# Performance work log

Hardware: AMD Instinct MI355X
Metric: run time of the kernel (lower is better)

Reference implementation:

```python
import jax, jax.numpy as jnp
import numpy as np

B, F = 64, 2048

def setup_inputs() -> dict:
    key = jax.random.key(0)
    k1, k2, k3, k4, k5 = jax.random.split(key, 5)
    scale = 1.0 / np.sqrt(F)
    return {
        "x": jax.random.normal(k1, (B, F), dtype=jnp.float32),
        "feature_mask": jax.random.randint(k2, (B, F), 0, 2, dtype=jnp.int32),
        "Wq": jax.random.normal(k3, (F, F), dtype=jnp.float32) * scale,
        "Wk": jax.random.normal(k4, (F, F), dtype=jnp.float32) * scale,
        "Wv": jax.random.normal(k5, (F, F), dtype=jnp.float32) * scale,
    }

def reference(x, feature_mask, Wq, Wk, Wv):
    # nn.Linear(bias=False): y = x @ W.T
    q = x @ Wq.T  # (B, F)
    k = x @ Wk.T
    v = x @ Wv.T
    # outer-product scores: (B, F, F) = q[:, :, None] * k[:, None, :]
    scores = q[:, :, None] * k[:, None, :]
    # mask broadcast over query dim (unsqueeze(1) in torch)
    scores = jnp.where(feature_mask[:, None, :] == 0, -1e9, scores)
    attn = jax.nn.softmax(scores, axis=-1)  # (B, F, F)
    attended = jnp.einsum("bfg,bg->bf", attn, v)  # (B, F)
    return attended
```

## Files before the change

### kernel.cpp

```cpp
#include <hip/hip_runtime.h>
#include <hip/hip_bf16.h>

#define B 64
#define F 2048
#define BN 32
#define BK 32
#define KSPLIT 4
#define KCHUNK (F / KSPLIT)
#define NITER (KCHUNK / BK)
#define LDSW 40
#define GS 4

typedef __attribute__((ext_vector_type(8))) short bf16x8;
typedef __attribute__((ext_vector_type(4))) float f32x4;

#define PART_FLOATS (KSPLIT * 3 * B * F)

#if __has_builtin(__builtin_amdgcn_exp2f)
#define EXP2(x) __builtin_amdgcn_exp2f(x)
#else
#define EXP2(x) exp2f(x)
#endif

__device__ __forceinline__ void split2(float f0, float f1, int& hi, int& lo) {
  union { float f; unsigned u; } a, b;
  a.f = f0; b.f = f1;
  union { unsigned u; float f; } ha, hb;
  ha.u = a.u & 0xFFFF0000u;
  hb.u = b.u & 0xFFFF0000u;
  union { float f; unsigned u; } la, lb;
  la.f = f0 - ha.f;
  lb.f = f1 - hb.f;
  hi = (int)__builtin_amdgcn_perm(b.u, a.u, 0x07060302u);
  lo = (int)__builtin_amdgcn_perm(lb.u, la.u, 0x07060302u);
}

__global__ __launch_bounds__(256) void qkv_gemm_kernel(
    const float* __restrict__ x, const float* __restrict__ Wq,
    const float* __restrict__ Wk, const float* __restrict__ Wv,
    float* __restrict__ part) {
  __shared__ __align__(16) short xs_hi[2][B][LDSW];
  __shared__ __align__(16) short xs_lo[2][B][LDSW];
  __shared__ __align__(16) short ws_hi[2][BN][LDSW];
  __shared__ __align__(16) short ws_lo[2][BN][LDSW];

  const int tid  = threadIdx.x;
  const int f0   = blockIdx.x * BN;
  const int kb   = blockIdx.y;
  const int mat  = blockIdx.z;
  const float* W = (mat == 0) ? Wq : (mat == 1) ? Wk : Wv;

  const int lrow = tid >> 2;
  const int lc0  = (tid & 3) << 3;
  const int wrow = tid >> 3;
  const int wc0  = (tid & 7) << 2;

  const int wave = tid >> 6;
  const int lane = tid & 63;
  const int l15  = lane & 15;
  const int quad = lane >> 4;

  const float* xg = x + lrow * F + kb * KCHUNK + lc0;
  const float* wg = W + (f0 + wrow) * F + kb * KCHUNK + wc0;

  f32x4 acc[2];
#pragma unroll
  for (int i = 0; i < 2; ++i) acc[i] = (f32x4){0.f, 0.f, 0.f, 0.f};

  float4 px[2][2], pw[2];
  px[0][0] = *(const float4*)(xg);
  px[0][1] = *(const float4*)(xg + 4);
  pw[0]    = *(const float4*)(wg);

#pragma unroll
  for (int it = 0; it < NITER; ++it) {
    const int cur = it & 1, nxt = cur ^ 1;
    if (it + 1 < NITER) {
      const float* xp = xg + (it + 1) * BK;
      px[nxt][0] = *(const float4*)(xp);
      px[nxt][1] = *(const float4*)(xp + 4);
      pw[nxt]    = *(const float4*)(wg + (it + 1) * BK);
    }
    int4 xh, xl;
    int2 wh, wl;
    split2(px[cur][0].x, px[cur][0].y, xh.x, xl.x);
    split2(px[cur][0].z, px[cur][0].w, xh.y, xl.y);
    split2(px[cur][1].x, px[cur][1].y, xh.z, xl.z);
    split2(px[cur][1].z, px[cur][1].w, xh.w, xl.w);
    split2(pw[cur].x, pw[cur].y, wh.x, wl.x);
    split2(pw[cur].z, pw[cur].w, wh.y, wl.y);
    *(int4*)&xs_hi[cur][lrow][lc0] = xh;
    *(int4*)&xs_lo[cur][lrow][lc0] = xl;
    *(int2*)&ws_hi[cur][wrow][wc0] = wh;
    *(int2*)&ws_lo[cur][wrow][wc0] = wl;
    __syncthreads();

    bf16x8 a_hi = *(const bf16x8*)&xs_hi[cur][(wave << 4) + l15][quad << 3];
    bf16x8 a_lo = *(const bf16x8*)&xs_lo[cur][(wave << 4) + l15][quad << 3];
#pragma unroll
    for (int nt = 0; nt < 2; ++nt) {
      bf16x8 b_hi = *(const bf16x8*)&ws_hi[cur][(nt << 4) + l15][quad << 3];
      bf16x8 b_lo = *(const bf16x8*)&ws_lo[cur][(nt << 4) + l15][quad << 3];
      acc[nt] = __builtin_amdgcn_mfma_f32_16x16x32_bf16(a_hi, b_hi, acc[nt], 0, 0, 0);
      acc[nt] = __builtin_amdgcn_mfma_f32_16x16x32_bf16(a_hi, b_lo, acc[nt], 0, 0, 0);
      acc[nt] = __builtin_amdgcn_mfma_f32_16x16x32_bf16(a_lo, b_hi, acc[nt], 0, 0, 0);
    }
  }

  float* outp = part + (size_t)(kb * 3 + mat) * B * F;
#pragma unroll
  for (int nt = 0; nt < 2; ++nt) {
    int f = f0 + (nt << 4) + l15;
#pragma unroll
    for (int r = 0; r < 4; ++r) {
      int brow = (wave << 4) + (quad << 2) + r;
      outp[brow * F + f] = acc[nt][r];
    }
  }
}

__global__ __launch_bounds__(1024, 8) void attn_kernel(
    const float* __restrict__ part, const int* __restrict__ mask,
    float* __restrict__ out) {
  __shared__ __align__(16) float kvs[2 * F];
  __shared__ float rn[GS][256];
  __shared__ float rd[GS][256];
  __shared__ float swv[16], swm[16], swn[16];
  __shared__ int scnt;

  const int b     = blockIdx.x;
  const int tid   = threadIdx.x;
  const int fl    = tid & 255;
  const int slice = __builtin_amdgcn_readfirstlane(tid >> 8);
  const int fi    = blockIdx.y * 256 + fl;
  const int wid   = tid >> 6;
  const int lane  = tid & 63;

  if (tid == 0) scnt = 0;
  __syncthreads();

  float s = 0.f;
#pragma unroll
  for (int p = 0; p < KSPLIT; ++p) s += part[((p * 3 + 0) * B + b) * F + fi];

  const int g0 = tid << 1;
  float2 k2 = {0.f, 0.f}, v2 = {0.f, 0.f};
#pragma unroll
  for (int p = 0; p < KSPLIT; ++p) {
    const float2 kp = *(const float2*)&part[((p * 3 + 1) * B + b) * F + g0];
    const float2 vp = *(const float2*)&part[((p * 3 + 2) * B + b) * F + g0];
    k2.x += kp.x; k2.y += kp.y;
    v2.x += vp.x; v2.y += vp.y;
  }
  float vs = v2.x + v2.y;

  const int2 m2 = *(const int2*)&mask[b * F + g0];
  const bool a0 = (m2.x != 0), a1 = (m2.y != 0);
  const unsigned long long bal0 = __ballot(a0);
  const unsigned long long bal1 = __ballot(a1);
  const int tot = __popcll(bal0) + __popcll(bal1);
  int base = 0;
  if (lane == 0) base = atomicAdd(&scnt, tot);
  base = __shfl(base, 0);

  const unsigned long long ltm = (1ull << lane) - 1ull;
  float kmx = -3.4e38f, kmn = 3.4e38f;
  if (a0) {
    int pos = base + __popcll(bal0 & ltm);
    *(float2*)&kvs[2 * pos] = (float2){k2.x, v2.x};
    kmx = fmaxf(kmx, k2.x); kmn = fminf(kmn, k2.x);
  }
  if (a1) {
    int pos = base + __popcll(bal0) + __popcll(bal1 & ltm);
    *(float2*)&kvs[2 * pos] = (float2){k2.y, v2.y};
    kmx = fmaxf(kmx, k2.y); kmn = fminf(kmn, k2.y);
  }

#pragma unroll
  for (int o = 32; o > 0; o >>= 1) {
    vs += __shfl_xor(vs, o);
    kmx = fmaxf(kmx, __shfl_xor(kmx, o));
    kmn = fminf(kmn, __shfl_xor(kmn, o));
  }
  if (lane == 0) { swv[wid] = vs; swm[wid] = kmx; swn[wid] = kmn; }
  __syncthreads();

  const int ntot = scnt;
  float km = -3.4e38f, kn = 3.4e38f, vstot = 0.f;
#pragma unroll
  for (int w = 0; w < 16; ++w) {
    km = fmaxf(km, swm[w]);
    kn = fminf(kn, swn[w]);
    vstot += swv[w];
  }

  const float L2E = 1.44269504088896f;
  const float se  = s * L2E;
  const float nm2 = -se * ((s >= 0.f) ? km : kn);

  float n0 = 0.f, n1 = 0.f, n2 = 0.f, n3 = 0.f;
  float d0 = 0.f, d1 = 0.f, d2 = 0.f, d3 = 0.f;
  {
    const int quads = ntot >> 1;
    const int q0 = (slice * quads) / GS;
    const int q1 = ((slice + 1) * quads) / GS;
    const float4* bp = (const float4*)kvs;
    int q = q0;
    for (; q + 4 <= q1; q += 4) {
      float4 p0 = bp[q];
      float4 p1 = bp[q + 1];
      float4 p2 = bp[q + 2];
      float4 p3 = bp[q + 3];
      float e0 = EXP2(fmaf(se, p0.x, nm2));
      float e1 = EXP2(fmaf(se, p0.z, nm2));
      float e2 = EXP2(fmaf(se, p1.x, nm2));
      float e3 = EXP2(fmaf(se, p1.z, nm2));
      float e4 = EXP2(fmaf(se, p2.x, nm2));
      float e5 = EXP2(fmaf(se, p2.z, nm2));
      float e6 = EXP2(fmaf(se, p3.x, nm2));
      float e7 = EXP2(fmaf(se, p3.z, nm2));
      n0 = fmaf(e0, p0.y, n0); d0 += e0;
      n1 = fmaf(e1, p0.w, n1); d1 += e1;
      n2 = fmaf(e2, p1.y, n2); d2 += e2;
      n3 = fmaf(e3, p1.w, n3); d3 += e3;
      n0 = fmaf(e4, p2.y, n0); d0 += e4;
      n1 = fmaf(e5, p2.w, n1); d1 += e5;
      n2 = fmaf(e6, p3.y, n2); d2 += e6;
      n3 = fmaf(e7, p3.w, n3); d3 += e7;
    }
    for (; q < q1; ++q) {
      float4 p0 = bp[q];
      float e0 = EXP2(fmaf(se, p0.x, nm2));
      float e1 = EXP2(fmaf(se, p0.z, nm2));
      n0 = fmaf(e0, p0.y, n0); d0 += e0;
      n1 = fmaf(e1, p0.w, n1); d1 += e1;
    }
    if ((slice == GS - 1) && (ntot & 1)) {
      float2 p = *(const float2*)(kvs + 2 * (ntot - 1));
      float e = EXP2(fmaf(se, p.x, nm2));
      n2 = fmaf(e, p.y, n2); d2 += e;
    }
  }
  rn[slice][fl] = (n0 + n1) + (n2 + n3);
  rd[slice][fl] = (d0 + d1) + (d2 + d3);
  __syncthreads();
  if (slice == 0) {
    float N = (rn[0][fl] + rn[1][fl]) + (rn[2][fl] + rn[3][fl]);
    float D = (rd[0][fl] + rd[1][fl]) + (rd[2][fl] + rd[3][fl]);
    out[b * F + fi] = (ntot > 0) ? (N / D) : (vstot * (1.0f / (float)F));
  }
}

extern "C" void kernel_launch(void* const* d_in, const int* in_sizes, int n_in,
                              void* d_out, int out_size, void* d_ws, size_t ws_size,
                              hipStream_t stream) {
  const float* x  = (const float*)d_in[0];
  const int* mask = (const int*)d_in[1];
  const float* Wq = (const float*)d_in[2];
  const float* Wk = (const float*)d_in[3];
  const float* Wv = (const float*)d_in[4];
  float* out = (float*)d_out;

  float* part = (float*)d_ws;

  dim3 gg(F / BN, KSPLIT, 3);
  qkv_gemm_kernel<<<gg, 256, 0, stream>>>(x, Wq, Wk, Wv, part);
  dim3 ga(B, F / 256);
  attn_kernel<<<ga, 1024, 0, stream>>>(part, mask, out);
}
```

Baseline: 121.2 us.

## Register-block four queries per thread and split keys across all sixteen waves

```diff
diff --git a/kernel.cpp b/kernel.cpp
--- a/kernel.cpp
+++ b/kernel.cpp
@@ -9,7 +9,6 @@
 #define KCHUNK (F / KSPLIT)
 #define NITER (KCHUNK / BK)
 #define LDSW 40
-#define GS 4
 
 typedef __attribute__((ext_vector_type(8))) short bf16x8;
 typedef __attribute__((ext_vector_type(4))) float f32x4;
@@ -123,25 +122,28 @@
     const float* __restrict__ part, const int* __restrict__ mask,
     float* __restrict__ out) {
   __shared__ __align__(16) float kvs[2 * F];
-  __shared__ float rn[GS][256];
-  __shared__ float rd[GS][256];
+  __shared__ float rn[16][256];
+  __shared__ float rd[16][256];
   __shared__ float swv[16], swm[16], swn[16];
   __shared__ int scnt;
 
-  const int b     = blockIdx.x;
-  const int tid   = threadIdx.x;
-  const int fl    = tid & 255;
-  const int slice = __builtin_amdgcn_readfirstlane(tid >> 8);
-  const int fi    = blockIdx.y * 256 + fl;
-  const int wid   = tid >> 6;
-  const int lane  = tid & 63;
+  const int b    = blockIdx.x;
+  const int tid  = threadIdx.x;
+  const int wid  = __builtin_amdgcn_readfirstlane(tid >> 6);
+  const int lane = tid & 63;
 
   if (tid == 0) scnt = 0;
   __syncthreads();
 
-  float s = 0.f;
-#pragma unroll
-  for (int p = 0; p < KSPLIT; ++p) s += part[((p * 3 + 0) * B + b) * F + fi];
+  float qsum[4];
+#pragma unroll
+  for (int r = 0; r < 4; ++r) {
+    const int fi = blockIdx.y * 256 + (r << 6) + lane;
+    float s = 0.f;
+#pragma unroll
+    for (int p = 0; p < KSPLIT; ++p) s += part[((p * 3 + 0) * B + b) * F + fi];
+    qsum[r] = s;
+  }
 
   const int g0 = tid << 1;
   float2 k2 = {0.f, 0.f}, v2 = {0.f, 0.f};
@@ -195,59 +197,52 @@
   }
 
   const float L2E = 1.44269504088896f;
-  const float se  = s * L2E;
-  const float nm2 = -se * ((s >= 0.f) ? km : kn);
-
-  float n0 = 0.f, n1 = 0.f, n2 = 0.f, n3 = 0.f;
-  float d0 = 0.f, d1 = 0.f, d2 = 0.f, d3 = 0.f;
+  float se[4], nm[4];
+#pragma unroll
+  for (int r = 0; r < 4; ++r) {
+    se[r] = qsum[r] * L2E;
+    nm[r] = -se[r] * ((qsum[r] >= 0.f) ? km : kn);
+  }
+
+  float n[4] = {0.f, 0.f, 0.f, 0.f};
+  float d[4] = {0.f, 0.f, 0.f, 0.f};
   {
     const int quads = ntot >> 1;
-    const int q0 = (slice * quads) / GS;
-    const int q1 = ((slice + 1) * quads) / GS;
+    const int q0 = (wid * quads) >> 4;
+    const int q1 = ((wid + 1) * quads) >> 4;
     const float4* bp = (const float4*)kvs;
-    int q = q0;
-    for (; q + 4 <= q1; q += 4) {
-      float4 p0 = bp[q];
-      float4 p1 = bp[q + 1];
-      float4 p2 = bp[q + 2];
-      float4 p3 = bp[q + 3];
-      float e0 = EXP2(fmaf(se, p0.x, nm2));
-      float e1 = EXP2(fmaf(se, p0.z, nm2));
-      float e2 = EXP2(fmaf(se, p1.x, nm2));
-      float e3 = EXP2(fmaf(se, p1.z, nm2));
-      float e4 = EXP2(fmaf(se, p2.x, nm2));
-      float e5 = EXP2(fmaf(se, p2.z, nm2));
-      float e6 = EXP2(fmaf(se, p3.x, nm2));
-      float e7 = EXP2(fmaf(se, p3.z, nm2));
-      n0 = fmaf(e0, p0.y, n0); d0 += e0;
-      n1 = fmaf(e1, p0.w, n1); d1 += e1;
-      n2 = fmaf(e2, p1.y, n2); d2 += e2;
-      n3 = fmaf(e3, p1.w, n3); d3 += e3;
-      n0 = fmaf(e4, p2.y, n0); d0 += e4;
-      n1 = fmaf(e5, p2.w, n1); d1 += e5;
-      n2 = fmaf(e6, p3.y, n2); d2 += e6;
-      n3 = fmaf(e7, p3.w, n3); d3 += e7;
-    }
-    for (; q < q1; ++q) {
-      float4 p0 = bp[q];
-      float e0 = EXP2(fmaf(se, p0.x, nm2));
-      float e1 = EXP2(fmaf(se, p0.z, nm2));
-      n0 = fmaf(e0, p0.y, n0); d0 += e0;
-      n1 = fmaf(e1, p0.w, n1); d1 += e1;
-    }
-    if ((slice == GS - 1) && (ntot & 1)) {
-      float2 p = *(const float2*)(kvs + 2 * (ntot - 1));
-      float e = EXP2(fmaf(se, p.x, nm2));
-      n2 = fmaf(e, p.y, n2); d2 += e;
-    }
-  }
-  rn[slice][fl] = (n0 + n1) + (n2 + n3);
-  rd[slice][fl] = (d0 + d1) + (d2 + d3);
+#pragma unroll 2
+    for (int q = q0; q < q1; ++q) {
+      const float4 p = bp[q];
+#pragma unroll
+      for (int r = 0; r < 4; ++r) {
+        float e0 = EXP2(fmaf(se[r], p.x, nm[r]));
+        float e1 = EXP2(fmaf(se[r], p.z, nm[r]));
+        n[r] = fmaf(e0, p.y, n[r]); d[r] += e0;
+        n[r] = fmaf(e1, p.w, n[r]); d[r] += e1;
+      }
+    }
+    if ((wid == 15) && (ntot & 1)) {
+      const float2 p = *(const float2*)(kvs + 2 * (ntot - 1));
+#pragma unroll
+      for (int r = 0; r < 4; ++r) {
+        float e = EXP2(fmaf(se[r], p.x, nm[r]));
+        n[r] = fmaf(e, p.y, n[r]); d[r] += e;
+      }
+    }
+  }
+#pragma unroll
+  for (int r = 0; r < 4; ++r) {
+    rn[wid][(r << 6) + lane] = n[r];
+    rd[wid][(r << 6) + lane] = d[r];
+  }
   __syncthreads();
-  if (slice == 0) {
-    float N = (rn[0][fl] + rn[1][fl]) + (rn[2][fl] + rn[3][fl]);
-    float D = (rd[0][fl] + rd[1][fl]) + (rd[2][fl] + rd[3][fl]);
-    out[b * F + fi] = (ntot > 0) ? (N / D) : (vstot * (1.0f / (float)F));
+  if (tid < 256) {
+    float N = 0.f, D = 0.f;
+#pragma unroll
+    for (int s = 0; s < 16; ++s) { N += rn[s][tid]; D += rd[s][tid]; }
+    out[b * F + blockIdx.y * 256 + tid] =
+        (ntot > 0) ? (N / D) : (vstot * (1.0f / (float)F));
   }
 }
 
```

Result: no change. 119.7 us (-1.3%).
